# Kernel optimization log

Hardware: AMD Instinct MI355X
Metric: run time of the kernel (lower is better)

## Reference

```python
import jax, jax.numpy as jnp
import numpy as np


def _component_indices(d, j):
    # Butterfly component at level j has block size k = d >> j.
    k = d >> j
    half = k // 2
    base = np.arange(d // k) * k                       # block starts
    p = (base[:, None] + np.arange(half)[None, :]).reshape(-1)  # [d//2]
    q = p + half
    return p, q


def butterfly_rotation(thetas, d):
    """Compose m = log2(d) butterfly components: R = B(d,d) @ B(d,d/2) @ ... @ B(d,2).
    thetas: [m, d//2] Givens angles per component (block-major order as in torch)."""
    m = thetas.shape[0]
    R = jnp.eye(d, dtype=thetas.dtype)
    for j in range(m):
        p, q = _component_indices(d, j)
        c = jnp.cos(thetas[j])
        s = jnp.sin(thetas[j])
        C = jnp.eye(d, dtype=thetas.dtype)
        C = C.at[p, p].set(c)
        C = C.at[q, q].set(c)
        C = C.at[p, q].set(-s)
        C = C.at[q, p].set(s)
        R = R @ C
    return R


def setup_inputs() -> dict:
    key = jax.random.key(0)
    ks = jax.random.split(key, 8)
    N, D_IN, D_OUT, R = 16384, 4096, 4096, 1024
    M = 10  # log2(R)
    return {
        "x": jax.random.normal(ks[0], (N, D_IN), dtype=jnp.float32),
        "W": jax.random.normal(ks[1], (D_OUT, D_IN), dtype=jnp.float32) * 0.02,
        "bias": jax.random.normal(ks[2], (D_OUT,), dtype=jnp.float32) * 0.02,
        "U": jax.random.normal(ks[3], (D_OUT, R), dtype=jnp.float32) * 0.02,
        "S": jax.random.uniform(ks[4], (R,), dtype=jnp.float32),
        "V": jax.random.normal(ks[5], (R, D_IN), dtype=jnp.float32) * 0.02,
        "thetas_u": jax.random.normal(ks[6], (M, R // 2), dtype=jnp.float32) * 0.1,
        "thetas_v": jax.random.normal(ks[7], (M, R // 2), dtype=jnp.float32) * 0.1,
    }


def reference(x, W, bias, U, S, V, thetas_u, thetas_v):
    r = S.shape[0]
    R_U = butterfly_rotation(thetas_u, r)  # [r, r]
    R_V = butterfly_rotation(thetas_v, r)  # [r, r]
    # base_layer(x)
    base = x @ W.T + bias                  # [N, out]
    # adapter: x @ V^T @ R_V @ diag(S) @ R_U^T @ U^T
    h = (x @ V.T) @ R_V                    # [N, r]
    h = h * S                              # diag(S)
    delta = (h @ R_U.T) @ U.T              # [N, out]
    return base + delta
```

## Files before the change

kernel.cpp:

```cpp
#include <hip/hip_runtime.h>
#include <cstdint>
#include <cstddef>


typedef __bf16 bf16x8 __attribute__((ext_vector_type(8)));
typedef float floatx4 __attribute__((ext_vector_type(4)));
typedef unsigned short ushortx8 __attribute__((ext_vector_type(8)));

__device__ __forceinline__ unsigned short f2bf(float f) {
    unsigned int u = __builtin_bit_cast(unsigned int, f);
    u += 0x7FFFu + ((u >> 16) & 1u);
    return (unsigned short)(u >> 16);
}

__device__ __forceinline__ void gld_lds16(const void* g, void* l) {
    __builtin_amdgcn_global_load_lds(
        (const __attribute__((address_space(1))) void*)g,
        (__attribute__((address_space(3))) void*)l,
        16, 0, 0);
}

__device__ __forceinline__ bf16x8 ldsv(const char* p) {
    return __builtin_bit_cast(bf16x8, *(const ushortx8*)p);
}

#define MFMA_BF16(a, b, c) __builtin_amdgcn_mfma_f32_16x16x32_bf16((a), (b), (c), 0, 0, 0)

__global__ __launch_bounds__(256) void butterfly_rows_kernel(
    const float* __restrict__ thetas_v, const float* __restrict__ thetas_u,
    const float* __restrict__ S,
    unsigned short* __restrict__ RVsb, unsigned short* __restrict__ RUb)
{
    const int d = 1024;
    __shared__ float w[1024];
    const int b   = blockIdx.x;
    const int mat = b >> 10;
    const int row = b & 1023;
    const float* th = mat ? thetas_u : thetas_v;
    const int t = threadIdx.x;

    for (int i = t; i < d; i += 256) w[i] = (i == row) ? 1.f : 0.f;
    __syncthreads();

    for (int j = 0; j < 10; ++j) {
        const int sh = 9 - j;
        const int halfm1 = (1 << sh) - 1;
        for (int i = t; i < d / 2; i += 256) {
            const int blk = i >> sh;
            const int off = i & halfm1;
            const int p = (blk << (sh + 1)) + off;
            const int q = p + (halfm1 + 1);
            const float theta = th[j * (d / 2) + i];
            float s, c;
            __sincosf(theta, &s, &c);
            const float wp = w[p], wq = w[q];
            w[p] = c * wp + s * wq;
            w[q] = -s * wp + c * wq;
        }
        __syncthreads();
    }

    if (mat == 0) {
        for (int i = t; i < d; i += 256) RVsb[row * d + i] = f2bf(w[i] * S[i]);
    } else {
        for (int i = t; i < d; i += 256) RUb[row * d + i] = f2bf(w[i]);
    }
}

__global__ __launch_bounds__(256) void cvt_f32_bf16_x8(
    const float* __restrict__ src, unsigned short* __restrict__ dst)
{
    const size_t i = ((size_t)blockIdx.x * 256 + threadIdx.x) * 8;
    float4 a = *(const float4*)(src + i);
    float4 b = *(const float4*)(src + i + 4);
    ushortx8 o;
    o[0] = f2bf(a.x); o[1] = f2bf(a.y); o[2] = f2bf(a.z); o[3] = f2bf(a.w);
    o[4] = f2bf(b.x); o[5] = f2bf(b.y); o[6] = f2bf(b.z); o[7] = f2bf(b.w);
    *(ushortx8*)(dst + i) = o;
}

__global__ __launch_bounds__(256) void transpose_to_bf16(
    const float* __restrict__ src, unsigned short* __restrict__ dst,
    int rows, int cols)
{
    __shared__ float tile[32][33];
    const int tx = threadIdx.x & 31, ty = threadIdx.x >> 5;
    const int c0 = blockIdx.x * 32, r0 = blockIdx.y * 32;
    for (int i = 0; i < 32; i += 8)
        tile[ty + i][tx] = src[(size_t)(r0 + ty + i) * cols + c0 + tx];
    __syncthreads();
    for (int i = 0; i < 32; i += 8)
        dst[(size_t)(c0 + ty + i) * rows + r0 + tx] = f2bf(tile[tx][ty + i]);
}

template <int EPI>
__global__ __launch_bounds__(256) void gemm_nt(
    const unsigned short* __restrict__ A,
    const unsigned short* __restrict__ B,
    float* __restrict__ Cf,
    unsigned short* __restrict__ Cb,
    const float* __restrict__ extra,
    int M, int N, int K)
{
    __shared__ __align__(16) unsigned short As[128 * 32];
    __shared__ __align__(16) unsigned short Bs[128 * 32];

    const int tid  = threadIdx.x;
    const int lane = tid & 63;
    const int wave = tid >> 6;
    const int wm = wave >> 1, wn = wave & 1;

    const int m0 = blockIdx.y * 128;
    const int n0 = blockIdx.x * 128;

    const int srow = wave * 32 + (lane >> 2);
    const int scol = (lane & 3) * 8;

    const unsigned short* gA = A + (size_t)(m0 + srow) * K + scol;
    const unsigned short* gB = B + (size_t)(n0 + srow) * K + scol;
    unsigned short* lA = As + wave * 32 * 32;
    unsigned short* lB = Bs + wave * 32 * 32;

    floatx4 acc[4][4];
#pragma unroll
    for (int i = 0; i < 4; ++i)
#pragma unroll
        for (int j = 0; j < 4; ++j) acc[i][j] = (floatx4)0.f;

    const int ar = lane & 15;
    const int ak = (lane >> 4) * 8;

    for (int kk = 0; kk < K; kk += 32) {
        gld_lds16(gA + kk, lA);
        gld_lds16(gA + kk + (size_t)16 * K, lA + 512);
        gld_lds16(gB + kk, lB);
        gld_lds16(gB + kk + (size_t)16 * K, lB + 512);
        __syncthreads();

        bf16x8 af[4], bfr[4];
#pragma unroll
        for (int tm = 0; tm < 4; ++tm)
            af[tm] = __builtin_bit_cast(bf16x8,
                *(const ushortx8*)&As[(wm * 64 + tm * 16 + ar) * 32 + ak]);
#pragma unroll
        for (int tn = 0; tn < 4; ++tn)
            bfr[tn] = __builtin_bit_cast(bf16x8,
                *(const ushortx8*)&Bs[(wn * 64 + tn * 16 + ar) * 32 + ak]);
#pragma unroll
        for (int tm = 0; tm < 4; ++tm)
#pragma unroll
            for (int tn = 0; tn < 4; ++tn)
                acc[tm][tn] = MFMA_BF16(af[tm], bfr[tn], acc[tm][tn]);
        __syncthreads();
    }

#pragma unroll
    for (int tm = 0; tm < 4; ++tm) {
#pragma unroll
        for (int tn = 0; tn < 4; ++tn) {
#pragma unroll
            for (int r = 0; r < 4; ++r) {
                const int row = m0 + wm * 64 + tm * 16 + (lane >> 4) * 4 + r;
                const int col = n0 + wn * 64 + tn * 16 + (lane & 15);
                const float v = acc[tm][tn][r];
                if (EPI == 1) {
                    Cf[(size_t)row * N + col] = v + extra[col];
                } else if (EPI == 2) {
                    Cb[(size_t)row * N + col] = f2bf(v);
                } else {
                    Cb[(size_t)row * N + col] = f2bf(v + extra[(size_t)row * N + col]);
                }
            }
        }
    }
}

template <int EPI>
__global__ __launch_bounds__(512, 2) void gemm256(
    const unsigned short* __restrict__ A,
    const unsigned short* __restrict__ B,
    float* __restrict__ Cf,
    unsigned short* __restrict__ Cb,
    const float* __restrict__ extra,
    int M, int N, int K, int swz_on)
{
    __shared__ __align__(16) unsigned short As[2][2][128][64];
    __shared__ __align__(16) unsigned short Bs[2][2][128][64];

    const int tid  = threadIdx.x;
    const int lane = tid & 63;
    const int wave = tid >> 6;
    const int wm = wave >> 2;
    const int wn = wave & 3;

    int bx = blockIdx.x, by = blockIdx.y;
    if (swz_on) {
        const int gx  = gridDim.x;
        const int nwg = gx * gridDim.y;
        const int f   = by * gx + bx;
        const int g   = (f & 7) * (nwg >> 3) + (f >> 3);
        bx = g % gx;
        by = g / gx;
    }
    const int m0 = by * 256;
    const int n0 = bx * 256;

    const int srow  = tid >> 3;
    const int scolb = (tid & 7) << 4;
    const int scol  = (scolb ^ ((srow & 7) << 4)) >> 1;
    const unsigned short* gA = A + (size_t)(m0 + srow) * K + scol;
    const unsigned short* gB = B + (size_t)(n0 + srow) * K + scol;
    char* lA = (char*)As + (wave << 10);
    char* lB = (char*)Bs + (wave << 10);
    const size_t rs64 = (size_t)64 * K;

    auto stA = [&](int t1, int h) {
        const unsigned short* s = gA + (size_t)h * 2 * rs64 + (size_t)t1 * 64;
        char* l = lA + (t1 & 1) * 32768 + h * 16384;
        gld_lds16(s, l);
        gld_lds16(s + rs64, l + 8192);
    };
    auto stB = [&](int t1, int h) {
        const unsigned short* s = gB + (size_t)h * 2 * rs64 + (size_t)t1 * 64;
        char* l = lB + (t1 & 1) * 32768 + h * 16384;
        gld_lds16(s, l);
        gld_lds16(s + rs64, l + 8192);
    };

    const int fr  = lane & 15;
    const int kg  = lane >> 4;
    const int swz = (fr & 7) << 4;
    const int ca0 = (kg << 4) ^ swz;
    const int ca1 = (64 + (kg << 4)) ^ swz;
    const int arb = (wm * 64 + fr) * 128;
    const int brb = (wn * 32 + fr) * 128;

    floatx4 acc[8][4];
#pragma unroll
    for (int i = 0; i < 8; ++i)
#pragma unroll
        for (int j = 0; j < 4; ++j) acc[i][j] = (floatx4)0.f;

    const int nkt = K >> 6;

    stA(0, 0); stB(0, 0); stB(0, 1); stA(0, 1);
    asm volatile("s_waitcnt vmcnt(4)" ::: "memory");
    __builtin_amdgcn_s_barrier();
    __builtin_amdgcn_sched_barrier(0);

    for (int t = 0; t < nkt; ++t) {
        const bool stg = (t + 1 < nkt);
        const char* Ad = (const char*)As + (t & 1) * 32768;
        const char* Bd = (const char*)Bs + (t & 1) * 32768;

        bf16x8 af[4][2], b0[2][2], b1[2][2];

#pragma unroll
        for (int mf = 0; mf < 4; ++mf) {
            af[mf][0] = ldsv(Ad + arb + mf * 2048 + ca0);
            af[mf][1] = ldsv(Ad + arb + mf * 2048 + ca1);
        }
#pragma unroll
        for (int nf = 0; nf < 2; ++nf) {
            b0[nf][0] = ldsv(Bd + brb + nf * 2048 + ca0);
            b0[nf][1] = ldsv(Bd + brb + nf * 2048 + ca1);
        }
        if (stg) { stA(t + 1, 0); asm volatile("s_waitcnt vmcnt(4)" ::: "memory"); }
        else     {                asm volatile("s_waitcnt vmcnt(2)" ::: "memory"); }
        __builtin_amdgcn_s_barrier();
        asm volatile("s_waitcnt lgkmcnt(0)" ::: "memory");
        __builtin_amdgcn_sched_barrier(0);
        __builtin_amdgcn_s_setprio(1);
#pragma unroll
        for (int mf = 0; mf < 4; ++mf)
#pragma unroll
            for (int nf = 0; nf < 2; ++nf) {
                acc[mf][nf] = MFMA_BF16(af[mf][0], b0[nf][0], acc[mf][nf]);
                acc[mf][nf] = MFMA_BF16(af[mf][1], b0[nf][1], acc[mf][nf]);
            }
        __builtin_amdgcn_s_setprio(0);
        __builtin_amdgcn_s_barrier();
        __builtin_amdgcn_sched_barrier(0);

#pragma unroll
        for (int nf = 0; nf < 2; ++nf) {
            b1[nf][0] = ldsv(Bd + 16384 + brb + nf * 2048 + ca0);
            b1[nf][1] = ldsv(Bd + 16384 + brb + nf * 2048 + ca1);
        }
        if (stg) { stB(t + 1, 0); asm volatile("s_waitcnt vmcnt(4)" ::: "memory"); }
        else     {                asm volatile("s_waitcnt vmcnt(0)" ::: "memory"); }
        __builtin_amdgcn_s_barrier();
        asm volatile("s_waitcnt lgkmcnt(0)" ::: "memory");
        __builtin_amdgcn_sched_barrier(0);
        __builtin_amdgcn_s_setprio(1);
#pragma unroll
        for (int mf = 0; mf < 4; ++mf)
#pragma unroll
            for (int nf = 0; nf < 2; ++nf) {
                acc[mf][2 + nf] = MFMA_BF16(af[mf][0], b1[nf][0], acc[mf][2 + nf]);
                acc[mf][2 + nf] = MFMA_BF16(af[mf][1], b1[nf][1], acc[mf][2 + nf]);
            }
        __builtin_amdgcn_s_setprio(0);
        __builtin_amdgcn_s_barrier();
        __builtin_amdgcn_sched_barrier(0);

#pragma unroll
        for (int mf = 0; mf < 4; ++mf) {
            af[mf][0] = ldsv(Ad + 16384 + arb + mf * 2048 + ca0);
            af[mf][1] = ldsv(Ad + 16384 + arb + mf * 2048 + ca1);
        }
        if (stg) stB(t + 1, 1);
        asm volatile("" ::: "memory");
        __builtin_amdgcn_s_barrier();
        asm volatile("s_waitcnt lgkmcnt(0)" ::: "memory");
        __builtin_amdgcn_sched_barrier(0);
        __builtin_amdgcn_s_setprio(1);
#pragma unroll
        for (int mf = 0; mf < 4; ++mf)
#pragma unroll
            for (int nf = 0; nf < 2; ++nf) {
                acc[4 + mf][2 + nf] = MFMA_BF16(af[mf][0], b1[nf][0], acc[4 + mf][2 + nf]);
                acc[4 + mf][2 + nf] = MFMA_BF16(af[mf][1], b1[nf][1], acc[4 + mf][2 + nf]);
            }
        __builtin_amdgcn_s_setprio(0);
        __builtin_amdgcn_s_barrier();
        __builtin_amdgcn_sched_barrier(0);

        if (stg) { stA(t + 1, 1); asm volatile("s_waitcnt vmcnt(4)" ::: "memory"); }
        else     {                asm volatile("" ::: "memory"); }
        __builtin_amdgcn_s_barrier();
        __builtin_amdgcn_sched_barrier(0);
        __builtin_amdgcn_s_setprio(1);
#pragma unroll
        for (int mf = 0; mf < 4; ++mf)
#pragma unroll
            for (int nf = 0; nf < 2; ++nf) {
                acc[4 + mf][nf] = MFMA_BF16(af[mf][0], b0[nf][0], acc[4 + mf][nf]);
                acc[4 + mf][nf] = MFMA_BF16(af[mf][1], b0[nf][1], acc[4 + mf][nf]);
            }
        __builtin_amdgcn_s_setprio(0);
        __builtin_amdgcn_s_barrier();
        __builtin_amdgcn_sched_barrier(0);
    }

    const int er4 = (lane >> 4) << 2;
    const int ec  = lane & 15;
#pragma unroll
    for (int Mq = 0; Mq < 2; ++Mq)
#pragma unroll
        for (int mf = 0; mf < 4; ++mf)
#pragma unroll
            for (int Nq = 0; Nq < 2; ++Nq)
#pragma unroll
                for (int nf = 0; nf < 2; ++nf)
#pragma unroll
                    for (int r = 0; r < 4; ++r) {
                        const int row = m0 + Mq * 128 + wm * 64 + mf * 16 + er4 + r;
                        const int col = n0 + Nq * 128 + wn * 32 + nf * 16 + ec;
                        const float v = acc[Mq * 4 + mf][Nq * 2 + nf][r];
                        if (EPI == 1) {
                            Cf[(size_t)row * N + col] = v + extra[col];
                        } else {
                            Cb[(size_t)row * N + col] = f2bf(v + extra[(size_t)row * N + col]);
                        }
                    }
    (void)M;
}

extern "C" void kernel_launch(void* const* d_in, const int* in_sizes, int n_in,
                              void* d_out, int out_size, void* d_ws, size_t ws_size,
                              hipStream_t stream)
{
    const int NB = 16384, DIN = 4096, DOUT = 4096, R = 1024;

    const float* x    = (const float*)d_in[0];
    const float* W    = (const float*)d_in[1];
    const float* bias = (const float*)d_in[2];
    const float* U    = (const float*)d_in[3];
    const float* S    = (const float*)d_in[4];
    const float* V    = (const float*)d_in[5];
    const float* th_u = (const float*)d_in[6];
    const float* th_v = (const float*)d_in[7];
    float* out = (float*)d_out;

    char* ws = (char*)d_ws;
    size_t off = 0;
    auto alloc = [&](size_t bytes) {
        char* p = ws + off;
        off += (bytes + 255) & ~(size_t)255;
        return p;
    };
    unsigned short* Xb   = (unsigned short*)alloc((size_t)NB * DIN * 2);
    unsigned short* Wctb = (unsigned short*)alloc((size_t)DOUT * DIN * 2);
    unsigned short* RVsb = (unsigned short*)alloc((size_t)R * R * 2);
    unsigned short* RUb  = (unsigned short*)alloc((size_t)R * R * 2);
    unsigned short* Tb   = (unsigned short*)alloc((size_t)R * R * 2);
    unsigned short* Ub   = (unsigned short*)alloc((size_t)DOUT * R * 2);
    unsigned short* Gb   = (unsigned short*)alloc((size_t)DOUT * R * 2);
    unsigned short* Vtb  = (unsigned short*)alloc((size_t)DIN * R * 2);
    if (off > ws_size) return;

    butterfly_rows_kernel<<<2048, 256, 0, stream>>>(th_v, th_u, S, RVsb, RUb);

    cvt_f32_bf16_x8<<<(NB * (size_t)DIN) / 2048, 256, 0, stream>>>(x, Xb);
    cvt_f32_bf16_x8<<<((size_t)DOUT * R) / 2048, 256, 0, stream>>>(U, Ub);
    transpose_to_bf16<<<dim3(DIN / 32, R / 32), 256, 0, stream>>>(V, Vtb, R, DIN);

    gemm_nt<2><<<dim3(R / 128, R / 128), 256, 0, stream>>>(
        RVsb, RUb, nullptr, Tb, nullptr, R, R, R);

    gemm_nt<2><<<dim3(R / 128, DOUT / 128), 256, 0, stream>>>(
        Ub, Tb, nullptr, Gb, nullptr, DOUT, R, R);

    gemm256<3><<<dim3(DIN / 256, DOUT / 256), 512, 0, stream>>>(
        Gb, Vtb, nullptr, Wctb, W, DOUT, DIN, R, 0);

    gemm256<1><<<dim3(DOUT / 256, NB / 256), 512, 0, stream>>>(
        Xb, Wctb, out, nullptr, bias, NB, DOUT, DIN, 1);
}
```

Measured before the change: 1.142 ms.

## Restructure GEMM main loop to prefetch A fragments and stage tiles further ahead

Rewrites the GEMM k-loop schedule so the first A-half of tile t+1 (and tile t+2's A global stage) is issued ahead, with A register fragments for the next iteration loaded at the end of the current one. It splits fragments into afA/afB sets, drops several barriers and lgkmcnt waits, and keeps about six outstanding global loads. The goal is more overlap of LDS and global loads with MFMA work and fewer synchronisation stalls. Past the last tile, the loads wrap to tile 0 as dummy loads, which adds traffic and some risk of LDS race hazards given the reduced barrier count.

```diff
diff --git a/kernel.cpp b/kernel.cpp
--- a/kernel.cpp
+++ b/kernel.cpp
@@ -25,6 +25,7 @@
 }
 
 #define MFMA_BF16(a, b, c) __builtin_amdgcn_mfma_f32_16x16x32_bf16((a), (b), (c), 0, 0, 0)
+#define SCHED0() __builtin_amdgcn_sched_barrier(0)
 
 __global__ __launch_bounds__(256) void butterfly_rows_kernel(
     const float* __restrict__ thetas_v, const float* __restrict__ thetas_u,
@@ -214,15 +215,15 @@
     char* lB = (char*)Bs + (wave << 10);
     const size_t rs64 = (size_t)64 * K;
 
-    auto stA = [&](int t1, int h) {
-        const unsigned short* s = gA + (size_t)h * 2 * rs64 + (size_t)t1 * 64;
-        char* l = lA + (t1 & 1) * 32768 + h * 16384;
+    auto stA = [&](int src_t, int dbuf, int h) {
+        const unsigned short* s = gA + (size_t)h * 2 * rs64 + (size_t)src_t * 64;
+        char* l = lA + dbuf * 32768 + h * 16384;
         gld_lds16(s, l);
         gld_lds16(s + rs64, l + 8192);
     };
-    auto stB = [&](int t1, int h) {
-        const unsigned short* s = gB + (size_t)h * 2 * rs64 + (size_t)t1 * 64;
-        char* l = lB + (t1 & 1) * 32768 + h * 16384;
+    auto stB = [&](int src_t, int dbuf, int h) {
+        const unsigned short* s = gB + (size_t)h * 2 * rs64 + (size_t)src_t * 64;
+        char* l = lB + dbuf * 32768 + h * 16384;
         gld_lds16(s, l);
         gld_lds16(s + rs64, l + 8192);
     };
@@ -243,104 +244,118 @@
 
     const int nkt = K >> 6;
 
-    stA(0, 0); stB(0, 0); stB(0, 1); stA(0, 1);
-    asm volatile("s_waitcnt vmcnt(4)" ::: "memory");
+    bf16x8 afA[4][2], afB[4][2], b0[2][2], b1[2][2];
+
+    stA(0, 0, 0); stB(0, 0, 0); stB(0, 0, 1); stA(0, 0, 1);
+    stA(1, 1, 0);
+    asm volatile("s_waitcnt vmcnt(6)" ::: "memory");
+    SCHED0();
     __builtin_amdgcn_s_barrier();
-    __builtin_amdgcn_sched_barrier(0);
+    SCHED0();
+    {
+        const char* Ad = (const char*)As;
+#pragma unroll
+        for (int mf = 0; mf < 4; ++mf) {
+            afA[mf][0] = ldsv(Ad + arb + mf * 2048 + ca0);
+            afA[mf][1] = ldsv(Ad + arb + mf * 2048 + ca1);
+        }
+    }
+    SCHED0();
 
     for (int t = 0; t < nkt; ++t) {
-        const bool stg = (t + 1 < nkt);
-        const char* Ad = (const char*)As + (t & 1) * 32768;
-        const char* Bd = (const char*)Bs + (t & 1) * 32768;
-
-        bf16x8 af[4][2], b0[2][2], b1[2][2];
-
-#pragma unroll
-        for (int mf = 0; mf < 4; ++mf) {
-            af[mf][0] = ldsv(Ad + arb + mf * 2048 + ca0);
-            af[mf][1] = ldsv(Ad + arb + mf * 2048 + ca1);
-        }
+        const int cb = t & 1, nb = cb ^ 1;
+        const char* Ad  = (const char*)As + cb * 32768;
+        const char* Bd  = (const char*)Bs + cb * 32768;
+        const char* Ad2 = (const char*)As + nb * 32768;
+        const int t1 = (t + 1 < nkt) ? t + 1 : 0;
+        const int t2 = (t + 2 < nkt) ? t + 2 : 0;
+
+        stB(t1, nb, 0);
+        asm volatile("s_waitcnt vmcnt(6)" ::: "memory");
+        SCHED0();
+        __builtin_amdgcn_s_barrier();
+        SCHED0();
 #pragma unroll
         for (int nf = 0; nf < 2; ++nf) {
             b0[nf][0] = ldsv(Bd + brb + nf * 2048 + ca0);
             b0[nf][1] = ldsv(Bd + brb + nf * 2048 + ca1);
         }
-        if (stg) { stA(t + 1, 0); asm volatile("s_waitcnt vmcnt(4)" ::: "memory"); }
-        else     {                asm volatile("s_waitcnt vmcnt(2)" ::: "memory"); }
-        __builtin_amdgcn_s_barrier();
-        asm volatile("s_waitcnt lgkmcnt(0)" ::: "memory");
-        __builtin_amdgcn_sched_barrier(0);
-        __builtin_amdgcn_s_setprio(1);
-#pragma unroll
-        for (int mf = 0; mf < 4; ++mf)
-#pragma unroll
-            for (int nf = 0; nf < 2; ++nf) {
-                acc[mf][nf] = MFMA_BF16(af[mf][0], b0[nf][0], acc[mf][nf]);
-                acc[mf][nf] = MFMA_BF16(af[mf][1], b0[nf][1], acc[mf][nf]);
-            }
-        __builtin_amdgcn_s_setprio(0);
-        __builtin_amdgcn_s_barrier();
-        __builtin_amdgcn_sched_barrier(0);
-
+        SCHED0();
 #pragma unroll
         for (int nf = 0; nf < 2; ++nf) {
             b1[nf][0] = ldsv(Bd + 16384 + brb + nf * 2048 + ca0);
             b1[nf][1] = ldsv(Bd + 16384 + brb + nf * 2048 + ca1);
         }
-        if (stg) { stB(t + 1, 0); asm volatile("s_waitcnt vmcnt(4)" ::: "memory"); }
-        else     {                asm volatile("s_waitcnt vmcnt(0)" ::: "memory"); }
+        SCHED0();
+        __builtin_amdgcn_s_setprio(1);
+#pragma unroll
+        for (int mf = 0; mf < 4; ++mf)
+#pragma unroll
+            for (int nf = 0; nf < 2; ++nf) {
+                acc[mf][nf] = MFMA_BF16(afA[mf][0], b0[nf][0], acc[mf][nf]);
+                acc[mf][nf] = MFMA_BF16(afA[mf][1], b0[nf][1], acc[mf][nf]);
+            }
+        __builtin_amdgcn_s_setprio(0);
+        SCHED0();
+
+        stB(t1, nb, 1);
+        asm volatile("s_waitcnt vmcnt(6)" ::: "memory");
+        SCHED0();
         __builtin_amdgcn_s_barrier();
-        asm volatile("s_waitcnt lgkmcnt(0)" ::: "memory");
-        __builtin_amdgcn_sched_barrier(0);
+        SCHED0();
+#pragma unroll
+        for (int mf = 0; mf < 4; ++mf) {
+            afB[mf][0] = ldsv(Ad + 16384 + arb + mf * 2048 + ca0);
+            afB[mf][1] = ldsv(Ad + 16384 + arb + mf * 2048 + ca1);
+        }
+        SCHED0();
         __builtin_amdgcn_s_setprio(1);
 #pragma unroll
         for (int mf = 0; mf < 4; ++mf)
 #pragma unroll
             for (int nf = 0; nf < 2; ++nf) {
-                acc[mf][2 + nf] = MFMA_BF16(af[mf][0], b1[nf][0], acc[mf][2 + nf]);
-                acc[mf][2 + nf] = MFMA_BF16(af[mf][1], b1[nf][1], acc[mf][2 + nf]);
+                acc[mf][2 + nf] = MFMA_BF16(afA[mf][0], b1[nf][0], acc[mf][2 + nf]);
+                acc[mf][2 + nf] = MFMA_BF16(afA[mf][1], b1[nf][1], acc[mf][2 + nf]);
             }
         __builtin_amdgcn_s_setprio(0);
+        SCHED0();
+
+        stA(t1, nb, 1);
+        SCHED0();
+        __builtin_amdgcn_s_setprio(1);
+#pragma unroll
+        for (int mf = 0; mf < 4; ++mf)
+#pragma unroll
+            for (int nf = 0; nf < 2; ++nf) {
+                acc[4 + mf][2 + nf] = MFMA_BF16(afB[mf][0], b1[nf][0], acc[4 + mf][2 + nf]);
+                acc[4 + mf][2 + nf] = MFMA_BF16(afB[mf][1], b1[nf][1], acc[4 + mf][2 + nf]);
+            }
+        __builtin_amdgcn_s_setprio(0);
+        SCHED0();
+
+        stA(t2, cb, 0);
+        asm volatile("s_waitcnt vmcnt(6)" ::: "memory");
+        SCHED0();
         __builtin_amdgcn_s_barrier();
-        __builtin_amdgcn_sched_barrier(0);
-
-#pragma unroll
-        for (int mf = 0; mf < 4; ++mf) {
-            af[mf][0] = ldsv(Ad + 16384 + arb + mf * 2048 + ca0);
-            af[mf][1] = ldsv(Ad + 16384 + arb + mf * 2048 + ca1);
-        }
-        if (stg) stB(t + 1, 1);
-        asm volatile("" ::: "memory");
-        __builtin_amdgcn_s_barrier();
-        asm volatile("s_waitcnt lgkmcnt(0)" ::: "memory");
-        __builtin_amdgcn_sched_barrier(0);
+        SCHED0();
+        if (t + 1 < nkt) {
+#pragma unroll
+            for (int mf = 0; mf < 4; ++mf) {
+                afA[mf][0] = ldsv(Ad2 + arb + mf * 2048 + ca0);
+                afA[mf][1] = ldsv(Ad2 + arb + mf * 2048 + ca1);
+            }
+        }
+        SCHED0();
         __builtin_amdgcn_s_setprio(1);
 #pragma unroll
         for (int mf = 0; mf < 4; ++mf)
 #pragma unroll
             for (int nf = 0; nf < 2; ++nf) {
-                acc[4 + mf][2 + nf] = MFMA_BF16(af[mf][0], b1[nf][0], acc[4 + mf][2 + nf]);
-                acc[4 + mf][2 + nf] = MFMA_BF16(af[mf][1], b1[nf][1], acc[4 + mf][2 + nf]);
+                acc[4 + mf][nf] = MFMA_BF16(afB[mf][0], b0[nf][0], acc[4 + mf][nf]);
+                acc[4 + mf][nf] = MFMA_BF16(afB[mf][1], b0[nf][1], acc[4 + mf][nf]);
             }
         __builtin_amdgcn_s_setprio(0);
-        __builtin_amdgcn_s_barrier();
-        __builtin_amdgcn_sched_barrier(0);
-
-        if (stg) { stA(t + 1, 1); asm volatile("s_waitcnt vmcnt(4)" ::: "memory"); }
-        else     {                asm volatile("" ::: "memory"); }
-        __builtin_amdgcn_s_barrier();
-        __builtin_amdgcn_sched_barrier(0);
-        __builtin_amdgcn_s_setprio(1);
-#pragma unroll
-        for (int mf = 0; mf < 4; ++mf)
-#pragma unroll
-            for (int nf = 0; nf < 2; ++nf) {
-                acc[4 + mf][nf] = MFMA_BF16(af[mf][0], b0[nf][0], acc[4 + mf][nf]);
-                acc[4 + mf][nf] = MFMA_BF16(af[mf][1], b0[nf][1], acc[4 + mf][nf]);
-            }
-        __builtin_amdgcn_s_setprio(0);
-        __builtin_amdgcn_s_barrier();
-        __builtin_amdgcn_sched_barrier(0);
+        SCHED0();
     }
 
     const int er4 = (lane >> 4) << 2;
```

Result: no change. 1.128 ms (-1.2%).
